# Kernel tuning notes

Hardware: AMD Instinct MI355X
Metric: run time of the kernel (lower is better)

Reference implementation:

```python
import jax, jax.numpy as jnp
import numpy as np

HEAD_DIM = 64
GRID = 4
DS = 4
EPS = 1e-6


def conv1x1(x, w, b):
    # x: (B,C,H,W), w: (O,C), b: (O,)
    return jnp.einsum('bchw,oc->bohw', x, w) + b[None, :, None, None]


def setup_inputs() -> dict:
    key = jax.random.key(0)
    ks = jax.random.split(key, 12)
    B, N, C = 16, 4096, 256
    s = 0.02
    return {
        'x': jax.random.normal(ks[0], (B, N, C), dtype=jnp.float32),
        'w_qkv': s * jax.random.normal(ks[1], (3 * C, C), dtype=jnp.float32),
        'b_qkv': jnp.zeros((3 * C,), dtype=jnp.float32),
        'w_q': s * jax.random.normal(ks[2], (C, C), dtype=jnp.float32),
        'b_q': jnp.zeros((C,), dtype=jnp.float32),
        'w_kv': s * jax.random.normal(ks[3], (2 * C, C), dtype=jnp.float32),
        'b_kv': jnp.zeros((2 * C,), dtype=jnp.float32),
        'w_proj': s * jax.random.normal(ks[4], (C, C), dtype=jnp.float32),
        'b_proj': jnp.zeros((C,), dtype=jnp.float32),
        'gn_w': jnp.ones((C,), dtype=jnp.float32),
        'gn_b': jnp.zeros((C,), dtype=jnp.float32),
    }


def reference(x, w_qkv, b_qkv, w_q, b_q, w_kv, b_kv, w_proj, b_proj, gn_w, gn_b):
    B, N, C = x.shape
    H = W = int(np.sqrt(N))
    hd = HEAD_DIM
    nh = C // hd
    gs = GRID
    scale = hd ** -0.5

    xi = x.transpose(0, 2, 1).reshape(B, C, H, W)
    qkv = conv1x1(xi, w_qkv, b_qkv)  # (B,3C,H,W)

    # ---- grid-window attention (gs x gs windows) ----
    gh, gw = H // gs, W // gs
    qkv = qkv.reshape(B, 3, nh, hd, gh, gs, gw, gs)
    qkv = qkv.transpose(1, 0, 2, 4, 6, 5, 7, 3).reshape(3, -1, gs * gs, hd)
    q, k, v = qkv[0], qkv[1], qkv[2]  # (B*nh*gh*gw, gs*gs, hd)
    attn = jax.nn.softmax(jnp.einsum('wqd,wkd->wqk', q, k) * scale, axis=-1)
    grid_x = jnp.einsum('wqk,wkd->wqd', attn, v)
    grid_x = grid_x.reshape(B, nh, gh, gw, gs, gs, hd)
    grid_x = grid_x.transpose(0, 1, 6, 2, 4, 3, 5).reshape(B, C, H, W)

    # channels_first LayerNorm(x + grid_x)
    z = xi + grid_x
    u = z.mean(1, keepdims=True)
    s2 = ((z - u) ** 2).mean(1, keepdims=True)
    grid_x = gn_w[None, :, None, None] * ((z - u) / jnp.sqrt(s2 + EPS)) + gn_b[None, :, None, None]

    # ---- pooled global attention ----
    qg = conv1x1(grid_x, w_q, b_q).reshape(B, nh, hd, N).transpose(0, 1, 3, 2)  # (B,nh,N,hd)
    pooled = grid_x.reshape(B, C, H // DS, DS, W // DS, DS).mean(axis=(3, 5))
    kv = conv1x1(pooled, w_kv, b_kv).reshape(B, 2, nh, hd, -1).transpose(1, 0, 2, 4, 3)
    k, v = kv[0], kv[1]  # (B,nh,Np,hd)
    attn = jax.nn.softmax(jnp.einsum('bhqd,bhkd->bhqk', qg, k) * scale, axis=-1)
    global_x = jnp.einsum('bhqk,bhkd->bhqd', attn, v)
    global_x = global_x.transpose(0, 1, 3, 2).reshape(B, C, H, W) + grid_x

    out = conv1x1(global_x, w_proj, b_proj)
    return out.reshape(B, C, N).transpose(0, 2, 1)
```

## Files before the change

### kernel.cpp

```cpp
#include <hip/hip_runtime.h>
#include <cstddef>

#define SCALE 0.125f
#define LN_EPS 1e-6f

typedef __attribute__((ext_vector_type(8))) short bf16x8;
typedef __attribute__((ext_vector_type(4))) float f32x4;

__device__ __forceinline__ unsigned short f2bf(float f) {
    unsigned u = __float_as_uint(f);
    return (unsigned short)((u + 0x7FFFu + ((u >> 16) & 1u)) >> 16);
}
__device__ __forceinline__ unsigned pack2(float a, float b) {
    return (unsigned)f2bf(a) | ((unsigned)f2bf(b) << 16);
}
__device__ __forceinline__ float bflo(unsigned v) { return __uint_as_float(v << 16); }
__device__ __forceinline__ float bfhi(unsigned v) { return __uint_as_float(v & 0xFFFF0000u); }
__device__ __forceinline__ float bf2f(short s) { return __uint_as_float(((unsigned)(unsigned short)s) << 16); }

#define GLOAD16(gp, lp) __builtin_amdgcn_global_load_lds( \
    (const __attribute__((address_space(1))) void*)(gp),  \
    (__attribute__((address_space(3))) void*)(lp), 16, 0, 0)

__global__ __launch_bounds__(256) void k_castw(
    const float* __restrict__ wqkv, const float* __restrict__ wq,
    const float* __restrict__ wkv, const float* __restrict__ wproj,
    short* __restrict__ wb)
{
    const int blk = blockIdx.x;
    const float* src; size_t so, doff;
    if (blk < 96)       { src = wqkv;  so = (size_t)blk * 2048;         doff = 0; }
    else if (blk < 128) { src = wq;    so = (size_t)(blk - 96) * 2048;  doff = 196608; }
    else if (blk < 192) { src = wkv;   so = (size_t)(blk - 128) * 2048; doff = 262144; }
    else                { src = wproj; so = (size_t)(blk - 192) * 2048; doff = 393216; }
    const size_t idx = so + (size_t)threadIdx.x * 8;
    const float4 f0 = *(const float4*)(src + idx);
    const float4 f1 = *(const float4*)(src + idx + 4);
    uint4 o;
    o.x = pack2(f0.x, f0.y); o.y = pack2(f0.z, f0.w);
    o.z = pack2(f1.x, f1.y); o.w = pack2(f1.z, f1.w);
    *(uint4*)(wb + doff + idx) = o;
}

__global__ __launch_bounds__(256) void k_castx(
    const float* __restrict__ x, short* __restrict__ xb)
{
    const size_t i = ((size_t)blockIdx.x * 256 + threadIdx.x) * 8;
    const float4 f0 = *(const float4*)(x + i);
    const float4 f1 = *(const float4*)(x + i + 4);
    uint4 o;
    o.x = pack2(f0.x, f0.y); o.y = pack2(f0.z, f0.w);
    o.z = pack2(f1.x, f1.y); o.w = pack2(f1.z, f1.w);
    *(uint4*)(xb + i) = o;
}

template<int OUTMODE>
__global__ __launch_bounds__(256, 2) void k_gemm(
    const short* __restrict__ Asrc, const short* __restrict__ Bw,
    const float* __restrict__ bias, void* __restrict__ Cdst,
    short* __restrict__ Vdst, int ldc, int nbn)
{
    __shared__ short As[2][128 * 64];
    __shared__ short Bs[2][128 * 64];

    const int tid = threadIdx.x;
    const int q8 = gridDim.x >> 3;
    const int bid = (blockIdx.x & 7) * q8 + (blockIdx.x >> 3);
    const int bm = bid / nbn, bn = bid % nbn;
    const size_t m0 = (size_t)bm * 128, n0 = (size_t)bn * 128;
    const int wid = tid >> 6, lane = tid & 63;
    const int wr = wid >> 1, wc = wid & 1;
    const int g = lane >> 4, r = lane & 15;
    const int rowc = lane >> 3, gran = lane & 7;

    f32x4 acc[4][4];
    #pragma unroll
    for (int mi = 0; mi < 4; ++mi)
        #pragma unroll
        for (int nj = 0; nj < 4; ++nj) acc[mi][nj] = (f32x4)0.f;

    auto STAGE = [&](int kt, int bufi) {
        const int k0 = kt * 64;
        #pragma unroll
        for (int i = 0; i < 4; ++i) {
            const int rbase = wid * 32 + i * 8;
            const int row = rbase + rowc;
            const int sg = gran ^ (row & 7);
            GLOAD16(Asrc + (m0 + row) * 256 + k0 + sg * 8, &As[bufi][rbase * 64]);
            GLOAD16(Bw   + (n0 + row) * 256 + k0 + sg * 8, &Bs[bufi][rbase * 64]);
        }
    };

    auto COMPUTE = [&](int bufi) {
        #pragma unroll
        for (int ks = 0; ks < 2; ++ks) {
            const int ke = ks * 32 + g * 8;
            bf16x8 a[4], b[4];
            #pragma unroll
            for (int mi = 0; mi < 4; ++mi) {
                const int row = wr * 64 + mi * 16 + r;
                a[mi] = *(const bf16x8*)&As[bufi][row * 64 + (ke ^ ((row & 7) << 3))];
            }
            #pragma unroll
            for (int nj = 0; nj < 4; ++nj) {
                const int row = wc * 64 + nj * 16 + r;
                b[nj] = *(const bf16x8*)&Bs[bufi][row * 64 + (ke ^ ((row & 7) << 3))];
            }
            #pragma unroll
            for (int mi = 0; mi < 4; ++mi)
                #pragma unroll
                for (int nj = 0; nj < 4; ++nj)
                    acc[mi][nj] = __builtin_amdgcn_mfma_f32_16x16x32_bf16(
                        a[mi], b[nj], acc[mi][nj], 0, 0, 0);
        }
    };

    STAGE(0, 0);
    __syncthreads();
    #pragma unroll
    for (int kt = 0; kt < 4; ++kt) {
        const int cur = kt & 1;
        if (kt < 3) STAGE(kt + 1, cur ^ 1);
        COMPUTE(cur);
        __syncthreads();
    }

    #pragma unroll
    for (int nj = 0; nj < 4; ++nj) {
        const size_t col = n0 + wc * 64 + nj * 16 + r;
        const float bv = bias[col];
        #pragma unroll
        for (int mi = 0; mi < 4; ++mi) {
            const size_t row = m0 + wr * 64 + mi * 16 + g * 4;
            #pragma unroll
            for (int e = 0; e < 4; ++e) {
                const float v = acc[mi][nj][e] + bv;
                const size_t rr = row + e;
                if (OUTMODE == 0) ((float*)Cdst)[rr * ldc + col] = v;
                else if (OUTMODE == 1) ((short*)Cdst)[rr * ldc + col] = (short)f2bf(v);
                else {
                    const int colk = (int)col - 256;
                    if (colk < 0) ((short*)Cdst)[rr * 256 + col] = (short)f2bf(v);
                    else {
                        const int hh = colk >> 6, dd = colk & 63;
                        Vdst[((((rr >> 8) * 4 + hh) * 64 + dd) << 8) + (rr & 255)] = (short)f2bf(v);
                    }
                }
            }
        }
    }
}

__global__ __launch_bounds__(256) void k_win2(
    const short* __restrict__ qkvb, const float* __restrict__ x,
    const float* __restrict__ gnw, const float* __restrict__ gnb,
    short* __restrict__ lnb, short* __restrict__ pooledb)
{
    __shared__ float qk[16][772];
    __shared__ float sm[4][16][16];

    const int tid = threadIdx.x;
    const int blk = blockIdx.x;
    const int b = blk >> 8, win = blk & 255;
    const int ghi = win >> 4, gwi = win & 15;
    const size_t nb = (size_t)b * 4096;

    {
        const int t = tid >> 4, l16 = tid & 15;
        const int n = (ghi * 4 + (t >> 2)) * 64 + gwi * 4 + (t & 3);
        const short* gp = qkvb + (nb + n) * 768;
        #pragma unroll
        for (int j = 0; j < 6; ++j) {
            const int c16 = l16 + j * 16;
            const uint4 u = *(const uint4*)(gp + c16 * 8);
            float4 a, c;
            a.x = bflo(u.x); a.y = bfhi(u.x); a.z = bflo(u.y); a.w = bfhi(u.y);
            c.x = bflo(u.z); c.y = bfhi(u.z); c.z = bflo(u.w); c.w = bfhi(u.w);
            *(float4*)&qk[t][c16 * 8] = a;
            *(float4*)&qk[t][c16 * 8 + 4] = c;
        }
    }
    __syncthreads();

    {
        const int h = tid >> 6, q = (tid >> 2) & 15, r = tid & 3;
        float4 qv[16];
        const float4* qrow = (const float4*)&qk[q][h * 64];
        #pragma unroll
        for (int i = 0; i < 16; ++i) qv[i] = qrow[i];
        #pragma unroll
        for (int i = 0; i < 4; ++i) {
            const int kt = i * 4 + r;
            const float4* krow = (const float4*)&qk[kt][256 + h * 64];
            float acc = 0.f;
            #pragma unroll
            for (int c4 = 0; c4 < 16; ++c4) {
                const float4 kk = krow[c4];
                acc += qv[c4].x * kk.x + qv[c4].y * kk.y + qv[c4].z * kk.z + qv[c4].w * kk.w;
            }
            sm[h][q][kt] = acc * SCALE;
        }
    }
    __syncthreads();

    if (tid < 64) {
        const int h = tid >> 4, q = tid & 15;
        float4* sp = (float4*)&sm[h][q][0];
        float4 s0 = sp[0], s1 = sp[1], s2 = sp[2], s3 = sp[3];
        float m = fmaxf(fmaxf(fmaxf(fmaxf(s0.x, s0.y), fmaxf(s0.z, s0.w)),
                              fmaxf(fmaxf(s1.x, s1.y), fmaxf(s1.z, s1.w))),
                        fmaxf(fmaxf(fmaxf(s2.x, s2.y), fmaxf(s2.z, s2.w)),
                              fmaxf(fmaxf(s3.x, s3.y), fmaxf(s3.z, s3.w))));
        s0.x = __expf(s0.x - m); s0.y = __expf(s0.y - m); s0.z = __expf(s0.z - m); s0.w = __expf(s0.w - m);
        s1.x = __expf(s1.x - m); s1.y = __expf(s1.y - m); s1.z = __expf(s1.z - m); s1.w = __expf(s1.w - m);
        s2.x = __expf(s2.x - m); s2.y = __expf(s2.y - m); s2.z = __expf(s2.z - m); s2.w = __expf(s2.w - m);
        s3.x = __expf(s3.x - m); s3.y = __expf(s3.y - m); s3.z = __expf(s3.z - m); s3.w = __expf(s3.w - m);
        const float l = s0.x + s0.y + s0.z + s0.w + s1.x + s1.y + s1.z + s1.w
                      + s2.x + s2.y + s2.z + s2.w + s3.x + s3.y + s3.z + s3.w;
        const float inv = 1.f / l;
        s0.x *= inv; s0.y *= inv; s0.z *= inv; s0.w *= inv;
        s1.x *= inv; s1.y *= inv; s1.z *= inv; s1.w *= inv;
        s2.x *= inv; s2.y *= inv; s2.z *= inv; s2.w *= inv;
        s3.x *= inv; s3.y *= inv; s3.z *= inv; s3.w *= inv;
        sp[0] = s0; sp[1] = s1; sp[2] = s2; sp[3] = s3;
    }
    __syncthreads();

    {
        const int h = tid >> 6, d = tid & 63;
        float v[16];
        #pragma unroll
        for (int kt = 0; kt < 16; ++kt) v[kt] = qk[kt][512 + h * 64 + d];
        #pragma unroll
        for (int q = 0; q < 16; ++q) {
            const float4* sp = (const float4*)&sm[h][q][0];
            const float4 a0 = sp[0], a1 = sp[1], a2 = sp[2], a3 = sp[3];
            float o = a0.x * v[0] + a0.y * v[1] + a0.z * v[2] + a0.w * v[3]
                    + a1.x * v[4] + a1.y * v[5] + a1.z * v[6] + a1.w * v[7]
                    + a2.x * v[8] + a2.y * v[9] + a2.z * v[10] + a2.w * v[11]
                    + a3.x * v[12] + a3.y * v[13] + a3.z * v[14] + a3.w * v[15];
            const int n = (ghi * 4 + (q >> 2)) * 64 + gwi * 4 + (q & 3);
            const float xr = x[(nb + n) * 256 + h * 64 + d];
            qk[q][h * 64 + d] = o + xr;
        }
    }
    __syncthreads();

    {
        const int wv = tid >> 6, lane = tid & 63;
        const float4 gw = ((const float4*)gnw)[lane];
        const float4 gb = ((const float4*)gnb)[lane];
        #pragma unroll
        for (int i = 0; i < 4; ++i) {
            const int t = wv * 4 + i;
            const float4 zv = *(const float4*)&qk[t][lane * 4];
            float ssum = zv.x + zv.y + zv.z + zv.w;
            for (int off = 1; off < 64; off <<= 1) ssum += __shfl_xor(ssum, off);
            const float u = ssum * (1.f / 256.f);
            const float dx = zv.x - u, dy = zv.y - u, dz = zv.z - u, dw = zv.w - u;
            float vsum = dx * dx + dy * dy + dz * dz + dw * dw;
            for (int off = 1; off < 64; off <<= 1) vsum += __shfl_xor(vsum, off);
            const float rinv = rsqrtf(vsum * (1.f / 256.f) + LN_EPS);
            float4 y;
            y.x = gw.x * dx * rinv + gb.x;
            y.y = gw.y * dy * rinv + gb.y;
            y.z = gw.z * dz * rinv + gb.z;
            y.w = gw.w * dw * rinv + gb.w;
            *(float4*)&qk[t][lane * 4] = y;
            const int n = (ghi * 4 + (t >> 2)) * 64 + gwi * 4 + (t & 3);
            short4 sv;
            sv.x = (short)f2bf(y.x); sv.y = (short)f2bf(y.y);
            sv.z = (short)f2bf(y.z); sv.w = (short)f2bf(y.w);
            *(short4*)(lnb + (nb + n) * 256 + lane * 4) = sv;
        }
    }
    __syncthreads();

    {
        float ps = 0.f;
        #pragma unroll
        for (int t = 0; t < 16; ++t) ps += qk[t][tid];
        pooledb[((size_t)b * 256 + win) * 256 + tid] = (short)f2bf(ps * (1.f / 16.f));
    }
}

#define CP 280
__global__ __launch_bounds__(512, 1) void k_glb(
    const short* __restrict__ qgb, const short* __restrict__ kb,
    const short* __restrict__ vtb, const short* __restrict__ lnb,
    short* __restrict__ gxb)
{
    __shared__ short Ks[256 * 64];
    __shared__ short Vt[64 * 256];
    __shared__ short Pl[8][16 * CP];

    const int tid = threadIdx.x;
    const int bid = (blockIdx.x & 7) * 256 + (blockIdx.x >> 3);
    const int bh = bid >> 5, qt = bid & 31;
    const int b = bh >> 2, h = bh & 3;
    const int q0 = qt * 128;
    const size_t nb = (size_t)b * 4096;

    #pragma unroll
    for (int i = 0; i < 4; ++i) {
        const int c = i * 512 + tid;
        const int p = c >> 3, d8 = (c & 7) * 8;
        const uint4 u = *(const uint4*)(kb + ((size_t)(b * 256 + p)) * 256 + h * 64 + d8);
        *(uint4*)&Ks[p * 64 + (d8 ^ ((p & 7) << 3))] = u;
    }
    const short* vsrc = vtb + (size_t)bh * 16384;
    #pragma unroll
    for (int i = 0; i < 4; ++i) {
        const int c = i * 512 + tid;
        const int d = c >> 5, k8 = (c & 31) * 8;
        const uint4 u = *(const uint4*)(vsrc + d * 256 + k8);
        *(uint4*)&Vt[d * 256 + (k8 ^ ((d & 7) << 3))] = u;
    }
    __syncthreads();

    const int w = tid >> 6, lane = tid & 63;
    const int g = lane >> 4, l15 = lane & 15;

    bf16x8 aq[2];
    {
        const int n = q0 + w * 16 + l15;
        const short* qp = qgb + (nb + n) * 256 + h * 64 + g * 8;
        aq[0] = *(const bf16x8*)qp;
        aq[1] = *(const bf16x8*)(qp + 32);
    }

    f32x4 acc[16];
    #pragma unroll
    for (int nt = 0; nt < 16; ++nt) acc[nt] = (f32x4)0.f;

    #pragma unroll
    for (int nt = 0; nt < 16; ++nt) {
        const int key = nt * 16 + l15;
        const int sw = (key & 7) << 3;
        const bf16x8 bk0 = *(const bf16x8*)&Ks[key * 64 + ((g * 8) ^ sw)];
        const bf16x8 bk1 = *(const bf16x8*)&Ks[key * 64 + ((g * 8 + 32) ^ sw)];
        acc[nt] = __builtin_amdgcn_mfma_f32_16x16x32_bf16(aq[0], bk0, acc[nt], 0, 0, 0);
        acc[nt] = __builtin_amdgcn_mfma_f32_16x16x32_bf16(aq[1], bk1, acc[nt], 0, 0, 0);
    }

    float rs[4];
    short* Pw = &Pl[w][0];
    #pragma unroll
    for (int e = 0; e < 4; ++e) {
        const int prow = (g * 4 + e) * CP;
        float rsum = 0.f;
        #pragma unroll
        for (int nt = 0; nt < 16; ++nt) {
            const float p = __expf(acc[nt][e] * SCALE);
            rsum += p;
            Pw[prow + nt * 16 + l15] = (short)f2bf(p);
        }
        rs[e] = rsum;
    }
    #pragma unroll
    for (int e = 0; e < 4; ++e) {
        float v = rs[e];
        v += __shfl_xor(v, 1); v += __shfl_xor(v, 2);
        v += __shfl_xor(v, 4); v += __shfl_xor(v, 8);
        rs[e] = v;
    }

    f32x4 oc[4];
    #pragma unroll
    for (int nt = 0; nt < 4; ++nt) oc[nt] = (f32x4)0.f;

    #pragma unroll
    for (int ks = 0; ks < 8; ++ks) {
        const int kc = ks * 32 + g * 8;
        const bf16x8 a0 = *(const bf16x8*)&Pw[l15 * CP + kc];
        #pragma unroll
        for (int nt = 0; nt < 4; ++nt) {
            const int d = nt * 16 + l15;
            const bf16x8 bv = *(const bf16x8*)&Vt[d * 256 + (kc ^ ((d & 7) << 3))];
            oc[nt] = __builtin_amdgcn_mfma_f32_16x16x32_bf16(a0, bv, oc[nt], 0, 0, 0);
        }
    }

    #pragma unroll
    for (int e = 0; e < 4; ++e) {
        const float inv = 1.f / rs[e];
        const int n = q0 + w * 16 + g * 4 + e;
        const size_t base = (nb + n) * 256 + h * 64;
        #pragma unroll
        for (int nt = 0; nt < 4; ++nt) {
            const int d = nt * 16 + l15;
            gxb[base + d] = (short)f2bf(oc[nt][e] * inv + bf2f(lnb[base + d]));
        }
    }
}

extern "C" void kernel_launch(void* const* d_in, const int* in_sizes, int n_in,
                              void* d_out, int out_size, void* d_ws, size_t ws_size,
                              hipStream_t stream)
{
    (void)in_sizes; (void)n_in; (void)out_size; (void)ws_size;
    const float* x     = (const float*)d_in[0];
    const float* wqkv  = (const float*)d_in[1];
    const float* bqkv  = (const float*)d_in[2];
    const float* wq    = (const float*)d_in[3];
    const float* bq    = (const float*)d_in[4];
    const float* wkv   = (const float*)d_in[5];
    const float* bkv   = (const float*)d_in[6];
    const float* wproj = (const float*)d_in[7];
    const float* bproj = (const float*)d_in[8];
    const float* gnw   = (const float*)d_in[9];
    const float* gnb   = (const float*)d_in[10];
    float* out = (float*)d_out;

    char* wsb = (char*)d_ws;
    short* wb      = (short*)(wsb + 0);
    short* qkvb    = (short*)(wsb + 1048576);
    short* lnb     = (short*)(wsb + 101711872);
    short* qgb     = (short*)(wsb + 135266304);
    short* kb      = (short*)(wsb + 168820736);
    short* vtb     = (short*)(wsb + 170917888);
    short* pooledb = (short*)(wsb + 173015040);
    short* gxb     = (short*)(wsb + 175112192);
    short* xb      = (short*)(wsb + 208666624);

    k_castw<<<dim3(224),  dim3(256), 0, stream>>>(wqkv, wq, wkv, wproj, wb);
    k_castx<<<dim3(8192), dim3(256), 0, stream>>>(x, xb);
    k_gemm<1><<<dim3(3072), dim3(256), 0, stream>>>(xb, wb, bqkv, qkvb, nullptr, 768, 6);
    k_win2<<<dim3(4096), dim3(256), 0, stream>>>(qkvb, x, gnw, gnb, lnb, pooledb);
    k_gemm<1><<<dim3(1024), dim3(256), 0, stream>>>(lnb, wb + 196608, bq, qgb, nullptr, 256, 2);
    k_gemm<2><<<dim3(128), dim3(256), 0, stream>>>(pooledb, wb + 262144, bkv, kb, vtb, 512, 4);
    k_glb<<<dim3(2048), dim3(512), 0, stream>>>(qgb, kb, vtb, lnb, gxb);
    k_gemm<0><<<dim3(1024), dim3(256), 0, stream>>>(gxb, wb + 393216, bproj, out, nullptr, 256, 2);
}
```

Measured before the change: 226.3 us.

## Use MFMA for window attention with pre-transposed V layout from QKV GEMM

The QKV GEMM gains an output mode that writes Q and K packed at stride 512 and scatters V into a per-window transposed layout. The window-attention kernel is rewritten to compute QK^T and PV with bf16 MFMA instructions, with softmax done through lane shuffles. The residual now reads the bf16 copy of x instead of fp32 x. This removes the fp32 LDS staging and scalar dot products, at the cost of a scattered V store in the GEMM epilogue and slightly lower residual precision.

```diff
diff --git a/kernel.cpp b/kernel.cpp
--- a/kernel.cpp
+++ b/kernel.cpp
@@ -138,122 +138,107 @@
                 const size_t rr = row + e;
                 if (OUTMODE == 0) ((float*)Cdst)[rr * ldc + col] = v;
                 else if (OUTMODE == 1) ((short*)Cdst)[rr * ldc + col] = (short)f2bf(v);
-                else {
+                else if (OUTMODE == 2) {
                     const int colk = (int)col - 256;
                     if (colk < 0) ((short*)Cdst)[rr * 256 + col] = (short)f2bf(v);
                     else {
                         const int hh = colk >> 6, dd = colk & 63;
                         Vdst[((((rr >> 8) * 4 + hh) * 64 + dd) << 8) + (rr & 255)] = (short)f2bf(v);
                     }
+                } else {
+                    if ((int)col < 512) ((short*)Cdst)[rr * 512 + col] = (short)f2bf(v);
+                    else {
+                        const int cc = (int)col - 512;
+                        const int hh = cc >> 6, dd = cc & 63;
+                        const int bb = (int)(rr >> 12), nn = (int)(rr & 4095);
+                        const int sr = nn >> 6, sc = nn & 63;
+                        const int wn = ((sr >> 2) << 4) + (sc >> 2);
+                        const int tk = ((sr & 3) << 2) + (sc & 3);
+                        Vdst[(((((size_t)bb * 256 + wn) * 4 + hh) * 64 + dd) << 4) + tk]
+                            = (short)f2bf(v);
+                    }
                 }
             }
         }
     }
 }
 
-__global__ __launch_bounds__(256) void k_win2(
-    const short* __restrict__ qkvb, const float* __restrict__ x,
-    const float* __restrict__ gnw, const float* __restrict__ gnb,
-    short* __restrict__ lnb, short* __restrict__ pooledb)
-{
-    __shared__ float qk[16][772];
-    __shared__ float sm[4][16][16];
+__global__ __launch_bounds__(256) void k_win3(
+    const short* __restrict__ qkvb, const short* __restrict__ vwb,
+    const short* __restrict__ xb, const float* __restrict__ gnw,
+    const float* __restrict__ gnb, short* __restrict__ lnb,
+    short* __restrict__ pooledb)
+{
+    __shared__ float zbuf[16][260];
+    __shared__ short Pb[4][16][40];
 
     const int tid = threadIdx.x;
     const int blk = blockIdx.x;
     const int b = blk >> 8, win = blk & 255;
     const int ghi = win >> 4, gwi = win & 15;
     const size_t nb = (size_t)b * 4096;
+    const int h = tid >> 6, lane = tid & 63;
+    const int g = lane >> 4, l15 = lane & 15;
+
+    const int n15 = (ghi * 4 + (l15 >> 2)) * 64 + gwi * 4 + (l15 & 3);
+    const size_t qkrow = (nb + n15) * 512;
+    const bf16x8 aq0 = *(const bf16x8*)(qkvb + qkrow + h * 64 + g * 8);
+    const bf16x8 aq1 = *(const bf16x8*)(qkvb + qkrow + h * 64 + 32 + g * 8);
+    const bf16x8 bk0 = *(const bf16x8*)(qkvb + qkrow + 256 + h * 64 + g * 8);
+    const bf16x8 bk1 = *(const bf16x8*)(qkvb + qkrow + 256 + h * 64 + 32 + g * 8);
+
+    f32x4 acc = (f32x4)0.f;
+    acc = __builtin_amdgcn_mfma_f32_16x16x32_bf16(aq0, bk0, acc, 0, 0, 0);
+    acc = __builtin_amdgcn_mfma_f32_16x16x32_bf16(aq1, bk1, acc, 0, 0, 0);
+
+    float p[4];
+    #pragma unroll
+    for (int e = 0; e < 4; ++e) {
+        const float s = acc[e] * SCALE;
+        float mm = s;
+        mm = fmaxf(mm, __shfl_xor(mm, 1)); mm = fmaxf(mm, __shfl_xor(mm, 2));
+        mm = fmaxf(mm, __shfl_xor(mm, 4)); mm = fmaxf(mm, __shfl_xor(mm, 8));
+        const float pe = __expf(s - mm);
+        float rs = pe;
+        rs += __shfl_xor(rs, 1); rs += __shfl_xor(rs, 2);
+        rs += __shfl_xor(rs, 4); rs += __shfl_xor(rs, 8);
+        p[e] = pe / rs;
+    }
+    #pragma unroll
+    for (int e = 0; e < 4; ++e) {
+        Pb[h][g * 4 + e][l15] = (short)f2bf(p[e]);
+        Pb[h][g * 4 + e][16 + l15] = 0;
+    }
+    __syncthreads();
+
+    const bf16x8 ap = *(const bf16x8*)&Pb[h][l15][g * 8];
+    f32x4 oc[4];
+    #pragma unroll
+    for (int nt = 0; nt < 4; ++nt) oc[nt] = (f32x4)0.f;
+    const short* vbase = vwb + ((((size_t)b * 256 + win) * 4 + h) << 10);
+    #pragma unroll
+    for (int nt = 0; nt < 4; ++nt) {
+        const bf16x8 bv = *(const bf16x8*)(vbase + (nt * 16 + l15) * 16 + g * 8);
+        oc[nt] = __builtin_amdgcn_mfma_f32_16x16x32_bf16(ap, bv, oc[nt], 0, 0, 0);
+    }
+    #pragma unroll
+    for (int e = 0; e < 4; ++e)
+        #pragma unroll
+        for (int nt = 0; nt < 4; ++nt)
+            zbuf[g * 4 + e][h * 64 + nt * 16 + l15] = oc[nt][e];
+    __syncthreads();
 
     {
-        const int t = tid >> 4, l16 = tid & 15;
-        const int n = (ghi * 4 + (t >> 2)) * 64 + gwi * 4 + (t & 3);
-        const short* gp = qkvb + (nb + n) * 768;
-        #pragma unroll
-        for (int j = 0; j < 6; ++j) {
-            const int c16 = l16 + j * 16;
-            const uint4 u = *(const uint4*)(gp + c16 * 8);
-            float4 a, c;
-            a.x = bflo(u.x); a.y = bfhi(u.x); a.z = bflo(u.y); a.w = bfhi(u.y);
-            c.x = bflo(u.z); c.y = bfhi(u.z); c.z = bflo(u.w); c.w = bfhi(u.w);
-            *(float4*)&qk[t][c16 * 8] = a;
-            *(float4*)&qk[t][c16 * 8 + 4] = c;
-        }
-    }
-    __syncthreads();
-
-    {
-        const int h = tid >> 6, q = (tid >> 2) & 15, r = tid & 3;
-        float4 qv[16];
-        const float4* qrow = (const float4*)&qk[q][h * 64];
-        #pragma unroll
-        for (int i = 0; i < 16; ++i) qv[i] = qrow[i];
-        #pragma unroll
-        for (int i = 0; i < 4; ++i) {
-            const int kt = i * 4 + r;
-            const float4* krow = (const float4*)&qk[kt][256 + h * 64];
-            float acc = 0.f;
-            #pragma unroll
-            for (int c4 = 0; c4 < 16; ++c4) {
-                const float4 kk = krow[c4];
-                acc += qv[c4].x * kk.x + qv[c4].y * kk.y + qv[c4].z * kk.z + qv[c4].w * kk.w;
-            }
-            sm[h][q][kt] = acc * SCALE;
-        }
-    }
-    __syncthreads();
-
-    if (tid < 64) {
-        const int h = tid >> 4, q = tid & 15;
-        float4* sp = (float4*)&sm[h][q][0];
-        float4 s0 = sp[0], s1 = sp[1], s2 = sp[2], s3 = sp[3];
-        float m = fmaxf(fmaxf(fmaxf(fmaxf(s0.x, s0.y), fmaxf(s0.z, s0.w)),
-                              fmaxf(fmaxf(s1.x, s1.y), fmaxf(s1.z, s1.w))),
-                        fmaxf(fmaxf(fmaxf(s2.x, s2.y), fmaxf(s2.z, s2.w)),
-                              fmaxf(fmaxf(s3.x, s3.y), fmaxf(s3.z, s3.w))));
-        s0.x = __expf(s0.x - m); s0.y = __expf(s0.y - m); s0.z = __expf(s0.z - m); s0.w = __expf(s0.w - m);
-        s1.x = __expf(s1.x - m); s1.y = __expf(s1.y - m); s1.z = __expf(s1.z - m); s1.w = __expf(s1.w - m);
-        s2.x = __expf(s2.x - m); s2.y = __expf(s2.y - m); s2.z = __expf(s2.z - m); s2.w = __expf(s2.w - m);
-        s3.x = __expf(s3.x - m); s3.y = __expf(s3.y - m); s3.z = __expf(s3.z - m); s3.w = __expf(s3.w - m);
-        const float l = s0.x + s0.y + s0.z + s0.w + s1.x + s1.y + s1.z + s1.w
-                      + s2.x + s2.y + s2.z + s2.w + s3.x + s3.y + s3.z + s3.w;
-        const float inv = 1.f / l;
-        s0.x *= inv; s0.y *= inv; s0.z *= inv; s0.w *= inv;
-        s1.x *= inv; s1.y *= inv; s1.z *= inv; s1.w *= inv;
-        s2.x *= inv; s2.y *= inv; s2.z *= inv; s2.w *= inv;
-        s3.x *= inv; s3.y *= inv; s3.z *= inv; s3.w *= inv;
-        sp[0] = s0; sp[1] = s1; sp[2] = s2; sp[3] = s3;
-    }
-    __syncthreads();
-
-    {
-        const int h = tid >> 6, d = tid & 63;
-        float v[16];
-        #pragma unroll
-        for (int kt = 0; kt < 16; ++kt) v[kt] = qk[kt][512 + h * 64 + d];
-        #pragma unroll
-        for (int q = 0; q < 16; ++q) {
-            const float4* sp = (const float4*)&sm[h][q][0];
-            const float4 a0 = sp[0], a1 = sp[1], a2 = sp[2], a3 = sp[3];
-            float o = a0.x * v[0] + a0.y * v[1] + a0.z * v[2] + a0.w * v[3]
-                    + a1.x * v[4] + a1.y * v[5] + a1.z * v[6] + a1.w * v[7]
-                    + a2.x * v[8] + a2.y * v[9] + a2.z * v[10] + a2.w * v[11]
-                    + a3.x * v[12] + a3.y * v[13] + a3.z * v[14] + a3.w * v[15];
-            const int n = (ghi * 4 + (q >> 2)) * 64 + gwi * 4 + (q & 3);
-            const float xr = x[(nb + n) * 256 + h * 64 + d];
-            qk[q][h * 64 + d] = o + xr;
-        }
-    }
-    __syncthreads();
-
-    {
-        const int wv = tid >> 6, lane = tid & 63;
         const float4 gw = ((const float4*)gnw)[lane];
         const float4 gb = ((const float4*)gnb)[lane];
         #pragma unroll
         for (int i = 0; i < 4; ++i) {
-            const int t = wv * 4 + i;
-            const float4 zv = *(const float4*)&qk[t][lane * 4];
+            const int t = h * 4 + i;
+            const int n = (ghi * 4 + (t >> 2)) * 64 + gwi * 4 + (t & 3);
+            float4 zv = *(const float4*)&zbuf[t][lane * 4];
+            const short4 xv = *(const short4*)(xb + (nb + n) * 256 + lane * 4);
+            zv.x += bf2f(xv.x); zv.y += bf2f(xv.y);
+            zv.z += bf2f(xv.z); zv.w += bf2f(xv.w);
             float ssum = zv.x + zv.y + zv.z + zv.w;
             for (int off = 1; off < 64; off <<= 1) ssum += __shfl_xor(ssum, off);
             const float u = ssum * (1.f / 256.f);
@@ -266,8 +251,7 @@
             y.y = gw.y * dy * rinv + gb.y;
             y.z = gw.z * dz * rinv + gb.z;
             y.w = gw.w * dw * rinv + gb.w;
-            *(float4*)&qk[t][lane * 4] = y;
-            const int n = (ghi * 4 + (t >> 2)) * 64 + gwi * 4 + (t & 3);
+            *(float4*)&zbuf[t][lane * 4] = y;
             short4 sv;
             sv.x = (short)f2bf(y.x); sv.y = (short)f2bf(y.y);
             sv.z = (short)f2bf(y.z); sv.w = (short)f2bf(y.w);
@@ -279,7 +263,7 @@
     {
         float ps = 0.f;
         #pragma unroll
-        for (int t = 0; t < 16; ++t) ps += qk[t][tid];
+        for (int t = 0; t < 16; ++t) ps += zbuf[t][tid];
         pooledb[((size_t)b * 256 + win) * 256 + tid] = (short)f2bf(ps * (1.f / 16.f));
     }
 }
@@ -415,6 +399,7 @@
     char* wsb = (char*)d_ws;
     short* wb      = (short*)(wsb + 0);
     short* qkvb    = (short*)(wsb + 1048576);
+    short* vwb     = (short*)(wsb + 68157440);
     short* lnb     = (short*)(wsb + 101711872);
     short* qgb     = (short*)(wsb + 135266304);
     short* kb      = (short*)(wsb + 168820736);
@@ -425,8 +410,8 @@
 
     k_castw<<<dim3(224),  dim3(256), 0, stream>>>(wqkv, wq, wkv, wproj, wb);
     k_castx<<<dim3(8192), dim3(256), 0, stream>>>(x, xb);
-    k_gemm<1><<<dim3(3072), dim3(256), 0, stream>>>(xb, wb, bqkv, qkvb, nullptr, 768, 6);
-    k_win2<<<dim3(4096), dim3(256), 0, stream>>>(qkvb, x, gnw, gnb, lnb, pooledb);
+    k_gemm<3><<<dim3(3072), dim3(256), 0, stream>>>(xb, wb, bqkv, qkvb, vwb, 512, 6);
+    k_win3<<<dim3(4096), dim3(256), 0, stream>>>(qkvb, vwb, xb, gnw, gnb, lnb, pooledb);
     k_gemm<1><<<dim3(1024), dim3(256), 0, stream>>>(lnb, wb + 196608, bq, qgb, nullptr, 256, 2);
     k_gemm<2><<<dim3(128), dim3(256), 0, stream>>>(pooledb, wb + 262144, bkv, kb, vtb, 512, 4);
     k_glb<<<dim3(2048), dim3(512), 0, stream>>>(qgb, kb, vtb, lnb, gxb);
```

Result: slower. 242.0 us (+6.9%).
